# Kernel tuning notes

Measured on AMD Instinct MI355X. Metric: run time of the kernel, lower is better.

Reference implementation:

```python
import jax, jax.numpy as jnp
import numpy as np
import math

BATCH, SEQ, HIDDEN, HEADS = 2, 2048, 1024, 16
HEAD_SIZE = HIDDEN // HEADS
NEG_INF = -10000.0  # faithful to the torch module's masking constant


def setup_inputs() -> dict:
    key = jax.random.key(0)
    k1, k2, k3, k4 = jax.random.split(key, 4)
    x = jax.random.normal(k1, (BATCH, SEQ, HIDDEN), dtype=jnp.float32)
    pos_table = jax.random.normal(k2, (SEQ, HIDDEN), dtype=jnp.float32) * 0.02
    # torch nn.Linear weight layout: [out_features, in_features]
    Wqkv = jax.random.normal(k3, (3 * HIDDEN, HIDDEN), dtype=jnp.float32) * (1.0 / math.sqrt(HIDDEN))
    Wout = jax.random.normal(k4, (HIDDEN, HIDDEN), dtype=jnp.float32) * (1.0 / math.sqrt(HIDDEN))
    return {"x": x, "pos_table": pos_table, "Wqkv": Wqkv, "Wout": Wout}


def reference(x, pos_table, Wqkv, Wout):
    b, n, h = x.shape
    # positional embedding added for Q/K projection only (V uses raw x)
    xp = x + pos_table[None, :n, :]
    qk = jnp.einsum('bnd,ed->bne', xp, Wqkv[: 2 * HIDDEN])          # [b, n, 2h]
    q, k = jnp.split(qk, 2, axis=-1)
    v = jnp.einsum('bnd,ed->bne', x, Wqkv[2 * HIDDEN:])             # [b, n, h]

    def to_heads(t):  # b n (h l) -> b h n l
        return t.reshape(b, n, HEADS, HEAD_SIZE).transpose(0, 2, 1, 3)

    q, k, v = to_heads(q), to_heads(k), to_heads(v)

    scores = jnp.einsum('bhql,bhkl->bhqk', q, k) / math.sqrt(HEAD_SIZE)
    q_ind = jnp.arange(n)[:, None]
    k_ind = jnp.arange(n)[None, :]
    mask = q_ind < k_ind                                            # True where future
    scores = jnp.where(mask, NEG_INF, scores)
    probs = jax.nn.softmax(scores, axis=-1)
    combined_v = jnp.einsum('bhqk,bhkl->bhql', probs, v)            # [b, h, n, l]
    combined_v = combined_v.transpose(0, 2, 1, 3).reshape(b, n, h)  # b h q l -> b q (h l)
    out = jnp.einsum('bnd,ed->bne', combined_v, Wout)
    return out
```

## Files before the change

kernel.cpp:

```cpp
#include <hip/hip_runtime.h>
#include <hip/hip_bf16.h>
#include <stdint.h>

#define BATCH 2
#define SEQ   2048
#define HID   1024
#define NHEAD 16
#define HD    64
#define MROWS (BATCH*SEQ)

typedef __attribute__((ext_vector_type(8))) short bf16x8;
typedef __attribute__((ext_vector_type(4))) float f32x4;

__device__ inline unsigned pk2(float a, float b){
  __hip_bfloat162 h = __float22bfloat162_rn(make_float2(a, b));
  union { __hip_bfloat162 h; unsigned u; } v; v.h = h;
  return v.u;
}
__device__ inline float fexp2(float x){
#if __has_builtin(__builtin_amdgcn_exp2f)
  return __builtin_amdgcn_exp2f(x);
#else
  return exp2f(x);
#endif
}
__device__ inline void lds_load16(const short* g, short* l){
  __builtin_amdgcn_global_load_lds(
      (const __attribute__((address_space(1))) void*)g,
      (__attribute__((address_space(3))) void*)l, 16, 0, 0);
}

__global__ __launch_bounds__(256) void cast_xpos(
    const float* __restrict__ x, const float* __restrict__ pos,
    short* __restrict__ xb, short* __restrict__ xv){
  int i = blockIdx.x * 256 + threadIdx.x;
  float4 xa = ((const float4*)x)[i];
  float4 pa = ((const float4*)pos)[i & (SEQ*HID/4 - 1)];
  uint2 sb, sv;
  sb.x = pk2(xa.x + pa.x, xa.y + pa.y);
  sb.y = pk2(xa.z + pa.z, xa.w + pa.w);
  sv.x = pk2(xa.x, xa.y);
  sv.y = pk2(xa.z, xa.w);
  ((uint2*)xb)[i] = sb;
  ((uint2*)xv)[i] = sv;
}

__global__ __launch_bounds__(256) void cast_w2(
    const float* __restrict__ w1, const float* __restrict__ w2,
    short* __restrict__ o1, short* __restrict__ o2){
  int i = blockIdx.x * 256 + threadIdx.x;
  const int n1 = 3*HID*HID/4;
  const float4* src; uint2* dst; int j;
  if (i < n1){ src = (const float4*)w1; dst = (uint2*)o1; j = i; }
  else       { src = (const float4*)w2; dst = (uint2*)o2; j = i - n1; }
  float4 a = src[j];
  uint2 s;
  s.x = pk2(a.x, a.y);
  s.y = pk2(a.z, a.w);
  dst[j] = s;
}

template<bool F32OUT>
__global__ __launch_bounds__(256) void gemm_bt(
    const short* __restrict__ A0, const short* __restrict__ A1, int split_bx,
    const short* __restrict__ W, void* __restrict__ Cout, int K, int ldc,
    int qsb, float qscale){
  __shared__ alignas(16) short As[2][128*32];
  __shared__ alignas(16) short Bs[2][128*32];
  const int bx = blockIdx.x, by = blockIdx.y;
  const short* A = (bx < split_bx) ? A0 : A1;
  const int tid  = threadIdx.x;
  const int w    = tid >> 6, lane = tid & 63;
  const int g    = lane >> 4, c = lane & 15;
  const int wr   = w >> 1, wc = w & 1;

  f32x4 acc[4][4];
#pragma unroll
  for (int m = 0; m < 4; ++m)
#pragma unroll
    for (int n = 0; n < 4; ++n) acc[m][n] = (f32x4){0.f, 0.f, 0.f, 0.f};

  const short* Abase = A + (size_t)(by*128) * K;
  const short* Wbase = W + (size_t)(bx*128) * K;

  auto stage = [&](int buf, int kt){
#pragma unroll
    for (int j = 0; j < 2; ++j){
      int ci  = w*128 + j*64 + lane;
      int row = ci >> 2, sub = ci & 3;
      lds_load16(Abase + (size_t)row*K + kt + sub*8, &As[buf][(w*128 + j*64)*8]);
      lds_load16(Wbase + (size_t)row*K + kt + sub*8, &Bs[buf][(w*128 + j*64)*8]);
    }
  };

  const int nk = K >> 5;
  stage(0, 0);
  int buf = 0;
  for (int ki = 0; ki < nk; ++ki){
    __syncthreads();
    if (ki + 1 < nk) stage(buf ^ 1, (ki + 1) * 32);

    bf16x8 af[4], bfr[4];
#pragma unroll
    for (int m = 0; m < 4; ++m)
      af[m] = *(const bf16x8*)&As[buf][(wr*64 + m*16 + c)*32 + g*8];
#pragma unroll
    for (int n = 0; n < 4; ++n)
      bfr[n] = *(const bf16x8*)&Bs[buf][(wc*64 + n*16 + c)*32 + g*8];
    __builtin_amdgcn_s_setprio(1);
#pragma unroll
    for (int m = 0; m < 4; ++m)
#pragma unroll
      for (int n = 0; n < 4; ++n)
        acc[m][n] = __builtin_amdgcn_mfma_f32_16x16x32_bf16(af[m], bfr[n], acc[m][n], 0, 0, 0);
    __builtin_amdgcn_s_setprio(0);
    buf ^= 1;
  }

  const float sc = (bx < qsb) ? qscale : 1.0f;
  const int row0 = by*128 + wr*64;
  const int col0 = bx*128 + wc*64;
#pragma unroll
  for (int m = 0; m < 4; ++m)
#pragma unroll
    for (int n = 0; n < 4; ++n){
      size_t base = (size_t)(row0 + m*16 + g*4) * ldc + (col0 + n*16 + c);
      if constexpr (F32OUT){
#pragma unroll
        for (int r = 0; r < 4; ++r)
          ((float*)Cout)[base + (size_t)r*ldc] = acc[m][n][r] * sc;
      } else {
        short* p = (short*)Cout + base;
        unsigned u01 = pk2(acc[m][n][0]*sc, acc[m][n][1]*sc);
        unsigned u23 = pk2(acc[m][n][2]*sc, acc[m][n][3]*sc);
        p[0]             = (short)(u01 & 0xffff);
        p[(size_t)ldc]   = (short)(u01 >> 16);
        p[2*(size_t)ldc] = (short)(u23 & 0xffff);
        p[3*(size_t)ldc] = (short)(u23 >> 16);
      }
    }
}

__global__ __launch_bounds__(256) void attn_fwd(
    const short* __restrict__ qkv, short* __restrict__ out){
  const int bid = blockIdx.x;
  const int qt  = 15 - (bid >> 5);
  const int bh  = bid & 31;
  const int b   = bh >> 4, h = bh & 15;
  const int tid = threadIdx.x;
  const int w   = tid >> 6, lane = tid & 63;
  const int g   = lane >> 4, c = lane & 15;

  __shared__ alignas(16) short Ks[2][64*64];
  __shared__ alignas(16) short Vt[2][64*64];

  const int q0 = qt*128 + w*32;
  const size_t rowb = (size_t)b * SEQ;

  const short* qptrA = qkv + (rowb + q0 + c)*3072 + h*HD;
  const short* qptrB = qptrA + 16*3072;
  bf16x8 qfA0 = *(const bf16x8*)(qptrA + g*8);
  bf16x8 qfA1 = *(const bf16x8*)(qptrA + 32 + g*8);
  bf16x8 qfB0 = *(const bf16x8*)(qptrB + g*8);
  bf16x8 qfB1 = *(const bf16x8*)(qptrB + 32 + g*8);

  const short* kbase = qkv + rowb*3072 + HID   + h*HD;
  const short* vbase = qkv + rowb*3072 + 2*HID + h*HD;

  const int slot   = ((lane >> 5) << 5) | (((lane >> 2) & 3) << 3)
                   | (((lane >> 4) & 1) << 2) | (lane & 3);
  const int vchunk = slot >> 3, vcol = slot & 7;

  auto stageK = [&](int buf, int c0){
#pragma unroll
    for (int j = 0; j < 2; ++j){
      int pc  = w*128 + j*64 + lane;
      int row = pc >> 3;
      int lc  = (pc & 7) ^ (row & 7);
      lds_load16(kbase + (size_t)(c0 + row)*3072 + lc*8, &Ks[buf][(w*128 + j*64)*8]);
    }
  };
  auto loadV = [&](int c0, bf16x8& v0, bf16x8& v1){
    const short* vp = vbase + (size_t)(c0 + lane)*3072 + w*16;
    v0 = *(const bf16x8*)(vp);
    v1 = *(const bf16x8*)(vp + 8);
  };
  auto scatterV = [&](int buf, const bf16x8& v0, const bf16x8& v1){
#pragma unroll
    for (int j = 0; j < 8; ++j)
      Vt[buf][(w*16 + j)*64 + ((vchunk ^ (j & 7)) << 3) + vcol] = v0[j];
#pragma unroll
    for (int j = 0; j < 8; ++j)
      Vt[buf][(w*16 + 8 + j)*64 + ((vchunk ^ ((8 + j) & 7)) << 3) + vcol] = v1[j];
  };

  f32x4 otA[4], otB[4];
#pragma unroll
  for (int dt = 0; dt < 4; ++dt){
    otA[dt] = (f32x4){0.f, 0.f, 0.f, 0.f};
    otB[dt] = (f32x4){0.f, 0.f, 0.f, 0.f};
  }
  float mA = -1e30f, lA = 0.f, mB = -1e30f, lB = 0.f;
  const int qgA = q0 + c, qgB = q0 + 16 + c;

  {
    bf16x8 v0, v1;
    stageK(0, 0);
    loadV(0, v0, v1);
    scatterV(0, v0, v1);
  }
  int cur = 0;
  const int nch = 2*qt + 2;
  for (int ch = 0; ch < nch; ++ch){
    const int c0 = ch * 64;
    __syncthreads();

    bf16x8 nv0, nv1;
    if (ch + 1 < nch){
      stageK(cur ^ 1, c0 + 64);
      loadV(c0 + 64, nv0, nv1);
    }

    if (c0 <= q0 + 31){
      f32x4 sA[4], sB[4];
      __builtin_amdgcn_s_setprio(1);
#pragma unroll
      for (int kt = 0; kt < 4; ++kt){
        int row = kt*16 + c;
        bf16x8 k0 = *(const bf16x8*)&Ks[cur][row*64 + ((g       ^ (row&7))<<3)];
        bf16x8 k1 = *(const bf16x8*)&Ks[cur][row*64 + (((4 + g) ^ (row&7))<<3)];
        f32x4 z = (f32x4){0.f, 0.f, 0.f, 0.f};
        sA[kt] = __builtin_amdgcn_mfma_f32_16x16x32_bf16(k0, qfA0, z, 0, 0, 0);
        sA[kt] = __builtin_amdgcn_mfma_f32_16x16x32_bf16(k1, qfA1, sA[kt], 0, 0, 0);
        sB[kt] = __builtin_amdgcn_mfma_f32_16x16x32_bf16(k0, qfB0, z, 0, 0, 0);
        sB[kt] = __builtin_amdgcn_mfma_f32_16x16x32_bf16(k1, qfB1, sB[kt], 0, 0, 0);
      }
      __builtin_amdgcn_s_setprio(0);

      float pa[16], pb[16];
#pragma unroll
      for (int kt = 0; kt < 4; ++kt)
#pragma unroll
        for (int r = 0; r < 4; ++r){
          pa[kt*4 + r] = sA[kt][r];
          pb[kt*4 + r] = sB[kt][r];
        }

      if (ch >= nch - 2){
#pragma unroll
        for (int kt = 0; kt < 4; ++kt)
#pragma unroll
          for (int r = 0; r < 4; ++r){
            int ki = c0 + kt*16 + g*4 + r;
            if (ki > qgA) pa[kt*4 + r] = -1e30f;
            if (ki > qgB) pb[kt*4 + r] = -1e30f;
          }
      }

      float cmA = fmaxf(fmaxf(fmaxf(pa[0], pa[1]),  fmaxf(pa[2],  pa[3])),
                        fmaxf(fmaxf(pa[4], pa[5]),  fmaxf(pa[6],  pa[7])));
      cmA = fmaxf(cmA, fmaxf(fmaxf(fmaxf(pa[8],  pa[9]),  fmaxf(pa[10], pa[11])),
                             fmaxf(fmaxf(pa[12], pa[13]), fmaxf(pa[14], pa[15]))));
      float cmB = fmaxf(fmaxf(fmaxf(pb[0], pb[1]),  fmaxf(pb[2],  pb[3])),
                        fmaxf(fmaxf(pb[4], pb[5]),  fmaxf(pb[6],  pb[7])));
      cmB = fmaxf(cmB, fmaxf(fmaxf(fmaxf(pb[8],  pb[9]),  fmaxf(pb[10], pb[11])),
                             fmaxf(fmaxf(pb[12], pb[13]), fmaxf(pb[14], pb[15]))));
      cmA = fmaxf(cmA, __shfl_xor(cmA, 16));
      cmA = fmaxf(cmA, __shfl_xor(cmA, 32));
      cmB = fmaxf(cmB, __shfl_xor(cmB, 16));
      cmB = fmaxf(cmB, __shfl_xor(cmB, 32));
      if (__any(cmA > mA + 8.0f)){
        float mnew  = fmaxf(mA, cmA);
        float alpha = fexp2(mA - mnew);
        lA *= alpha;
#pragma unroll
        for (int dt = 0; dt < 4; ++dt)
#pragma unroll
          for (int r = 0; r < 4; ++r) otA[dt][r] *= alpha;
        mA = mnew;
      }
      if (__any(cmB > mB + 8.0f)){
        float mnew  = fmaxf(mB, cmB);
        float alpha = fexp2(mB - mnew);
        lB *= alpha;
#pragma unroll
        for (int dt = 0; dt < 4; ++dt)
#pragma unroll
          for (int r = 0; r < 4; ++r) otB[dt][r] *= alpha;
        mB = mnew;
      }
      float psA = 0.f, psB = 0.f;
#pragma unroll
      for (int i = 0; i < 16; ++i){
        pa[i] = fexp2(pa[i] - mA); psA += pa[i];
        pb[i] = fexp2(pb[i] - mB); psB += pb[i];
      }
      psA += __shfl_xor(psA, 16); psA += __shfl_xor(psA, 32);
      psB += __shfl_xor(psB, 16); psB += __shfl_xor(psB, 32);
      lA += psA; lB += psB;

      union { unsigned u[4]; bf16x8 v; } pA0, pA1, pB0, pB1;
      pA0.u[0] = pk2(pa[0],  pa[1]);  pA0.u[1] = pk2(pa[2],  pa[3]);
      pA0.u[2] = pk2(pa[4],  pa[5]);  pA0.u[3] = pk2(pa[6],  pa[7]);
      pA1.u[0] = pk2(pa[8],  pa[9]);  pA1.u[1] = pk2(pa[10], pa[11]);
      pA1.u[2] = pk2(pa[12], pa[13]); pA1.u[3] = pk2(pa[14], pa[15]);
      pB0.u[0] = pk2(pb[0],  pb[1]);  pB0.u[1] = pk2(pb[2],  pb[3]);
      pB0.u[2] = pk2(pb[4],  pb[5]);  pB0.u[3] = pk2(pb[6],  pb[7]);
      pB1.u[0] = pk2(pb[8],  pb[9]);  pB1.u[1] = pk2(pb[10], pb[11]);
      pB1.u[2] = pk2(pb[12], pb[13]); pB1.u[3] = pk2(pb[14], pb[15]);

      __builtin_amdgcn_s_setprio(1);
#pragma unroll
      for (int dt = 0; dt < 4; ++dt){
        int d = dt*16 + c;
        bf16x8 va0 = *(const bf16x8*)&Vt[cur][d*64 + ((g       ^ (d&7))<<3)];
        bf16x8 va1 = *(const bf16x8*)&Vt[cur][d*64 + (((4 + g) ^ (d&7))<<3)];
        otA[dt] = __builtin_amdgcn_mfma_f32_16x16x32_bf16(va0, pA0.v, otA[dt], 0, 0, 0);
        otA[dt] = __builtin_amdgcn_mfma_f32_16x16x32_bf16(va1, pA1.v, otA[dt], 0, 0, 0);
        otB[dt] = __builtin_amdgcn_mfma_f32_16x16x32_bf16(va0, pB0.v, otB[dt], 0, 0, 0);
        otB[dt] = __builtin_amdgcn_mfma_f32_16x16x32_bf16(va1, pB1.v, otB[dt], 0, 0, 0);
      }
      __builtin_amdgcn_s_setprio(0);
    }

    if (ch + 1 < nch) scatterV(cur ^ 1, nv0, nv1);
    cur ^= 1;
  }

  float invA = 1.f / lA, invB = 1.f / lB;
  short* obA = out + (rowb + q0 + c)*HID + h*HD + g*4;
  short* obB = obA + 16*HID;
#pragma unroll
  for (int dt = 0; dt < 4; ++dt){
    uint2 ua, ub;
    ua.x = pk2(otA[dt][0]*invA, otA[dt][1]*invA);
    ua.y = pk2(otA[dt][2]*invA, otA[dt][3]*invA);
    ub.x = pk2(otB[dt][0]*invB, otB[dt][1]*invB);
    ub.y = pk2(otB[dt][2]*invB, otB[dt][3]*invB);
    *(uint2*)(obA + dt*16) = ua;
    *(uint2*)(obB + dt*16) = ub;
  }
}

extern "C" void kernel_launch(void* const* d_in, const int* in_sizes, int n_in,
                              void* d_out, int out_size, void* d_ws, size_t ws_size,
                              hipStream_t stream){
  const float* x    = (const float*)d_in[0];
  const float* pos  = (const float*)d_in[1];
  const float* Wqkv = (const float*)d_in[2];
  const float* Wout = (const float*)d_in[3];

  short* xb     = (short*)d_ws;
  short* xv     = xb    + (size_t)MROWS*HID;
  short* wqkvb  = xv    + (size_t)MROWS*HID;
  short* woutb  = wqkvb + (size_t)3*HID*HID;
  short* qkv    = woutb + (size_t)HID*HID;
  short* attn_o = xb;

  cast_xpos<<<dim3(MROWS*HID/1024), 256, 0, stream>>>(x, pos, xb, xv);
  cast_w2<<<dim3(4*HID*HID/1024), 256, 0, stream>>>(Wqkv, Wout, wqkvb, woutb);

  gemm_bt<false><<<dim3(24, 32), 256, 0, stream>>>(xb, xv, 16, wqkvb, qkv, HID, 3*HID,
                                                   8, 0.18033688011112042f);

  attn_fwd<<<dim3(512), 256, 0, stream>>>(qkv, attn_o);

  gemm_bt<true><<<dim3(8, 32), 256, 0, stream>>>(attn_o, attn_o, 8, woutb, d_out, HID, HID,
                                                 0, 1.0f);
}
```

Before: 213.0 us.

## Split attention KV range across two wave halves, drop online max, remap GEMM grid

The two cast kernels are merged into one launch. Both GEMMs switch to a 1D grid with an XCD-aware block remap. Attention blocks now use 512 threads, with each half processing a balanced share of KV chunks and the halves combined through LDS at the end. The running-max rescaling is removed and replaced by a fixed -16 offset in the score accumulator, which removes max reductions and rescale work but relies on the scores staying bounded for numerical safety.

```diff
diff --git a/kernel.cpp b/kernel.cpp
--- a/kernel.cpp
+++ b/kernel.cpp
@@ -30,44 +30,49 @@
       (__attribute__((address_space(3))) void*)l, 16, 0, 0);
 }
 
-__global__ __launch_bounds__(256) void cast_xpos(
+__global__ __launch_bounds__(256) void cast_all(
     const float* __restrict__ x, const float* __restrict__ pos,
-    short* __restrict__ xb, short* __restrict__ xv){
-  int i = blockIdx.x * 256 + threadIdx.x;
-  float4 xa = ((const float4*)x)[i];
-  float4 pa = ((const float4*)pos)[i & (SEQ*HID/4 - 1)];
-  uint2 sb, sv;
-  sb.x = pk2(xa.x + pa.x, xa.y + pa.y);
-  sb.y = pk2(xa.z + pa.z, xa.w + pa.w);
-  sv.x = pk2(xa.x, xa.y);
-  sv.y = pk2(xa.z, xa.w);
-  ((uint2*)xb)[i] = sb;
-  ((uint2*)xv)[i] = sv;
-}
-
-__global__ __launch_bounds__(256) void cast_w2(
     const float* __restrict__ w1, const float* __restrict__ w2,
+    short* __restrict__ xb, short* __restrict__ xv,
     short* __restrict__ o1, short* __restrict__ o2){
   int i = blockIdx.x * 256 + threadIdx.x;
-  const int n1 = 3*HID*HID/4;
-  const float4* src; uint2* dst; int j;
-  if (i < n1){ src = (const float4*)w1; dst = (uint2*)o1; j = i; }
-  else       { src = (const float4*)w2; dst = (uint2*)o2; j = i - n1; }
-  float4 a = src[j];
-  uint2 s;
-  s.x = pk2(a.x, a.y);
-  s.y = pk2(a.z, a.w);
-  dst[j] = s;
+  const int n0 = MROWS*HID/4;
+  if (i < n0){
+    float4 xa = ((const float4*)x)[i];
+    float4 pa = ((const float4*)pos)[i & (SEQ*HID/4 - 1)];
+    uint2 sb, sv;
+    sb.x = pk2(xa.x + pa.x, xa.y + pa.y);
+    sb.y = pk2(xa.z + pa.z, xa.w + pa.w);
+    sv.x = pk2(xa.x, xa.y);
+    sv.y = pk2(xa.z, xa.w);
+    ((uint2*)xb)[i] = sb;
+    ((uint2*)xv)[i] = sv;
+  } else {
+    int j = i - n0;
+    const int n1 = 3*HID*HID/4;
+    const float4* src; uint2* dst; int k;
+    if (j < n1){ src = (const float4*)w1; dst = (uint2*)o1; k = j; }
+    else       { src = (const float4*)w2; dst = (uint2*)o2; k = j - n1; }
+    float4 a = src[k];
+    uint2 s;
+    s.x = pk2(a.x, a.y);
+    s.y = pk2(a.z, a.w);
+    dst[k] = s;
+  }
 }
 
 template<bool F32OUT>
 __global__ __launch_bounds__(256) void gemm_bt(
     const short* __restrict__ A0, const short* __restrict__ A1, int split_bx,
     const short* __restrict__ W, void* __restrict__ Cout, int K, int ldc,
-    int qsb, float qscale){
+    int gx, int qsb, float qscale){
+  const int nwg  = gridDim.x;
+  const int q    = nwg >> 3;
+  const int wgid = (blockIdx.x % 8) * q + (blockIdx.x / 8);
+  const int bx = wgid % gx, by = wgid / gx;
+
   __shared__ alignas(16) short As[2][128*32];
   __shared__ alignas(16) short Bs[2][128*32];
-  const int bx = blockIdx.x, by = blockIdx.y;
   const short* A = (bx < split_bx) ? A0 : A1;
   const int tid  = threadIdx.x;
   const int w    = tid >> 6, lane = tid & 63;
@@ -141,20 +146,20 @@
     }
 }
 
-__global__ __launch_bounds__(256) void attn_fwd(
+__global__ __launch_bounds__(512, 4) void attn_fwd(
     const short* __restrict__ qkv, short* __restrict__ out){
   const int bid = blockIdx.x;
-  const int qt  = 15 - (bid >> 5);
+  const int s   = 15 - (bid >> 5);
   const int bh  = bid & 31;
   const int b   = bh >> 4, h = bh & 15;
   const int tid = threadIdx.x;
-  const int w   = tid >> 6, lane = tid & 63;
-  const int g   = lane >> 4, c = lane & 15;
-
-  __shared__ alignas(16) short Ks[2][64*64];
-  __shared__ alignas(16) short Vt[2][64*64];
-
-  const int q0 = qt*128 + w*32;
+  const int wv  = tid >> 6, w4 = wv & 3, hf = wv >> 2;
+  const int lane = tid & 63, g = lane >> 4, c = lane & 15;
+
+  __shared__ alignas(16) short Ks[2][2][64*64];
+  __shared__ alignas(16) short Vt[2][2][64*64];
+
+  const int q0 = s*128 + w4*32;
   const size_t rowb = (size_t)b * SEQ;
 
   const short* qptrA = qkv + (rowb + q0 + c)*3072 + h*HD;
@@ -174,24 +179,25 @@
   auto stageK = [&](int buf, int c0){
 #pragma unroll
     for (int j = 0; j < 2; ++j){
-      int pc  = w*128 + j*64 + lane;
+      int pc  = w4*128 + j*64 + lane;
       int row = pc >> 3;
       int lc  = (pc & 7) ^ (row & 7);
-      lds_load16(kbase + (size_t)(c0 + row)*3072 + lc*8, &Ks[buf][(w*128 + j*64)*8]);
+      lds_load16(kbase + (size_t)(c0 + row)*3072 + lc*8,
+                 &Ks[hf][buf][(w4*128 + j*64)*8]);
     }
   };
   auto loadV = [&](int c0, bf16x8& v0, bf16x8& v1){
-    const short* vp = vbase + (size_t)(c0 + lane)*3072 + w*16;
+    const short* vp = vbase + (size_t)(c0 + lane)*3072 + w4*16;
     v0 = *(const bf16x8*)(vp);
     v1 = *(const bf16x8*)(vp + 8);
   };
   auto scatterV = [&](int buf, const bf16x8& v0, const bf16x8& v1){
 #pragma unroll
     for (int j = 0; j < 8; ++j)
-      Vt[buf][(w*16 + j)*64 + ((vchunk ^ (j & 7)) << 3) + vcol] = v0[j];
+      Vt[hf][buf][(w4*16 + j)*64 + ((vchunk ^ (j & 7)) << 3) + vcol] = v0[j];
 #pragma unroll
     for (int j = 0; j < 8; ++j)
-      Vt[buf][(w*16 + 8 + j)*64 + ((vchunk ^ ((8 + j) & 7)) << 3) + vcol] = v1[j];
+      Vt[hf][buf][(w4*16 + 8 + j)*64 + ((vchunk ^ ((8 + j) & 7)) << 3) + vcol] = v1[j];
   };
 
   f32x4 otA[4], otB[4];
@@ -200,39 +206,41 @@
     otA[dt] = (f32x4){0.f, 0.f, 0.f, 0.f};
     otB[dt] = (f32x4){0.f, 0.f, 0.f, 0.f};
   }
-  float mA = -1e30f, lA = 0.f, mB = -1e30f, lB = 0.f;
+  float lrA = 0.f, lrB = 0.f;
   const int qgA = q0 + c, qgB = q0 + 16 + c;
+  const int dch = q0 >> 6;
+  const int base_ch = hf ? (s + 1) : 0;
 
   {
     bf16x8 v0, v1;
-    stageK(0, 0);
-    loadV(0, v0, v1);
+    stageK(0, base_ch*64);
+    loadV(base_ch*64, v0, v1);
     scatterV(0, v0, v1);
   }
   int cur = 0;
-  const int nch = 2*qt + 2;
-  for (int ch = 0; ch < nch; ++ch){
+  for (int i = 0; i <= s; ++i){
+    const int ch = base_ch + i;
     const int c0 = ch * 64;
     __syncthreads();
 
     bf16x8 nv0, nv1;
-    if (ch + 1 < nch){
+    if (i < s){
       stageK(cur ^ 1, c0 + 64);
       loadV(c0 + 64, nv0, nv1);
     }
 
-    if (c0 <= q0 + 31){
+    if (ch <= dch){
       f32x4 sA[4], sB[4];
+      const f32x4 zsh = (f32x4){-16.f, -16.f, -16.f, -16.f};
       __builtin_amdgcn_s_setprio(1);
 #pragma unroll
       for (int kt = 0; kt < 4; ++kt){
         int row = kt*16 + c;
-        bf16x8 k0 = *(const bf16x8*)&Ks[cur][row*64 + ((g       ^ (row&7))<<3)];
-        bf16x8 k1 = *(const bf16x8*)&Ks[cur][row*64 + (((4 + g) ^ (row&7))<<3)];
-        f32x4 z = (f32x4){0.f, 0.f, 0.f, 0.f};
-        sA[kt] = __builtin_amdgcn_mfma_f32_16x16x32_bf16(k0, qfA0, z, 0, 0, 0);
+        bf16x8 k0 = *(const bf16x8*)&Ks[hf][cur][row*64 + ((g       ^ (row&7))<<3)];
+        bf16x8 k1 = *(const bf16x8*)&Ks[hf][cur][row*64 + (((4 + g) ^ (row&7))<<3)];
+        sA[kt] = __builtin_amdgcn_mfma_f32_16x16x32_bf16(k0, qfA0, zsh, 0, 0, 0);
         sA[kt] = __builtin_amdgcn_mfma_f32_16x16x32_bf16(k1, qfA1, sA[kt], 0, 0, 0);
-        sB[kt] = __builtin_amdgcn_mfma_f32_16x16x32_bf16(k0, qfB0, z, 0, 0, 0);
+        sB[kt] = __builtin_amdgcn_mfma_f32_16x16x32_bf16(k0, qfB0, zsh, 0, 0, 0);
         sB[kt] = __builtin_amdgcn_mfma_f32_16x16x32_bf16(k1, qfB1, sB[kt], 0, 0, 0);
       }
       __builtin_amdgcn_s_setprio(0);
@@ -246,7 +254,7 @@
           pb[kt*4 + r] = sB[kt][r];
         }
 
-      if (ch >= nch - 2){
+      if (ch == dch){
 #pragma unroll
         for (int kt = 0; kt < 4; ++kt)
 #pragma unroll
@@ -257,47 +265,13 @@
           }
       }
 
-      float cmA = fmaxf(fmaxf(fmaxf(pa[0], pa[1]),  fmaxf(pa[2],  pa[3])),
-                        fmaxf(fmaxf(pa[4], pa[5]),  fmaxf(pa[6],  pa[7])));
-      cmA = fmaxf(cmA, fmaxf(fmaxf(fmaxf(pa[8],  pa[9]),  fmaxf(pa[10], pa[11])),
-                             fmaxf(fmaxf(pa[12], pa[13]), fmaxf(pa[14], pa[15]))));
-      float cmB = fmaxf(fmaxf(fmaxf(pb[0], pb[1]),  fmaxf(pb[2],  pb[3])),
-                        fmaxf(fmaxf(pb[4], pb[5]),  fmaxf(pb[6],  pb[7])));
-      cmB = fmaxf(cmB, fmaxf(fmaxf(fmaxf(pb[8],  pb[9]),  fmaxf(pb[10], pb[11])),
-                             fmaxf(fmaxf(pb[12], pb[13]), fmaxf(pb[14], pb[15]))));
-      cmA = fmaxf(cmA, __shfl_xor(cmA, 16));
-      cmA = fmaxf(cmA, __shfl_xor(cmA, 32));
-      cmB = fmaxf(cmB, __shfl_xor(cmB, 16));
-      cmB = fmaxf(cmB, __shfl_xor(cmB, 32));
-      if (__any(cmA > mA + 8.0f)){
-        float mnew  = fmaxf(mA, cmA);
-        float alpha = fexp2(mA - mnew);
-        lA *= alpha;
-#pragma unroll
-        for (int dt = 0; dt < 4; ++dt)
-#pragma unroll
-          for (int r = 0; r < 4; ++r) otA[dt][r] *= alpha;
-        mA = mnew;
-      }
-      if (__any(cmB > mB + 8.0f)){
-        float mnew  = fmaxf(mB, cmB);
-        float alpha = fexp2(mB - mnew);
-        lB *= alpha;
-#pragma unroll
-        for (int dt = 0; dt < 4; ++dt)
-#pragma unroll
-          for (int r = 0; r < 4; ++r) otB[dt][r] *= alpha;
-        mB = mnew;
-      }
       float psA = 0.f, psB = 0.f;
 #pragma unroll
-      for (int i = 0; i < 16; ++i){
-        pa[i] = fexp2(pa[i] - mA); psA += pa[i];
-        pb[i] = fexp2(pb[i] - mB); psB += pb[i];
-      }
-      psA += __shfl_xor(psA, 16); psA += __shfl_xor(psA, 32);
-      psB += __shfl_xor(psB, 16); psB += __shfl_xor(psB, 32);
-      lA += psA; lB += psB;
+      for (int i2 = 0; i2 < 16; ++i2){
+        pa[i2] = fexp2(pa[i2]); psA += pa[i2];
+        pb[i2] = fexp2(pb[i2]); psB += pb[i2];
+      }
+      lrA += psA; lrB += psB;
 
       union { unsigned u[4]; bf16x8 v; } pA0, pA1, pB0, pB1;
       pA0.u[0] = pk2(pa[0],  pa[1]);  pA0.u[1] = pk2(pa[2],  pa[3]);
@@ -313,8 +287,8 @@
 #pragma unroll
       for (int dt = 0; dt < 4; ++dt){
         int d = dt*16 + c;
-        bf16x8 va0 = *(const bf16x8*)&Vt[cur][d*64 + ((g       ^ (d&7))<<3)];
-        bf16x8 va1 = *(const bf16x8*)&Vt[cur][d*64 + (((4 + g) ^ (d&7))<<3)];
+        bf16x8 va0 = *(const bf16x8*)&Vt[hf][cur][d*64 + ((g       ^ (d&7))<<3)];
+        bf16x8 va1 = *(const bf16x8*)&Vt[hf][cur][d*64 + (((4 + g) ^ (d&7))<<3)];
         otA[dt] = __builtin_amdgcn_mfma_f32_16x16x32_bf16(va0, pA0.v, otA[dt], 0, 0, 0);
         otA[dt] = __builtin_amdgcn_mfma_f32_16x16x32_bf16(va1, pA1.v, otA[dt], 0, 0, 0);
         otB[dt] = __builtin_amdgcn_mfma_f32_16x16x32_bf16(va0, pB0.v, otB[dt], 0, 0, 0);
@@ -323,22 +297,52 @@
       __builtin_amdgcn_s_setprio(0);
     }
 
-    if (ch + 1 < nch) scatterV(cur ^ 1, nv0, nv1);
+    if (i < s) scatterV(cur ^ 1, nv0, nv1);
     cur ^= 1;
   }
 
-  float invA = 1.f / lA, invB = 1.f / lB;
-  short* obA = out + (rowb + q0 + c)*HID + h*HD + g*4;
-  short* obB = obA + 16*HID;
-#pragma unroll
-  for (int dt = 0; dt < 4; ++dt){
-    uint2 ua, ub;
-    ua.x = pk2(otA[dt][0]*invA, otA[dt][1]*invA);
-    ua.y = pk2(otA[dt][2]*invA, otA[dt][3]*invA);
-    ub.x = pk2(otB[dt][0]*invB, otB[dt][1]*invB);
-    ub.y = pk2(otB[dt][2]*invB, otB[dt][3]*invB);
-    *(uint2*)(obA + dt*16) = ua;
-    *(uint2*)(obB + dt*16) = ub;
+  __syncthreads();
+  float* CmbA = (float*)&Ks[0][0][0];
+  float* CmbB = (float*)&Vt[0][0][0];
+  if (hf){
+    float* pA = CmbA + (w4*64 + lane)*18;
+    float* pB = CmbB + (w4*64 + lane)*16;
+#pragma unroll
+    for (int dt = 0; dt < 4; ++dt)
+#pragma unroll
+      for (int r = 0; r < 4; ++r){
+        pA[dt*4 + r] = otA[dt][r];
+        pB[dt*4 + r] = otB[dt][r];
+      }
+    pA[16] = lrA; pA[17] = lrB;
+  }
+  __syncthreads();
+  if (!hf){
+    const float* pA = CmbA + (w4*64 + lane)*18;
+    const float* pB = CmbB + (w4*64 + lane)*16;
+#pragma unroll
+    for (int dt = 0; dt < 4; ++dt)
+#pragma unroll
+      for (int r = 0; r < 4; ++r){
+        otA[dt][r] += pA[dt*4 + r];
+        otB[dt][r] += pB[dt*4 + r];
+      }
+    lrA += pA[16]; lrB += pA[17];
+    lrA += __shfl_xor(lrA, 16); lrA += __shfl_xor(lrA, 32);
+    lrB += __shfl_xor(lrB, 16); lrB += __shfl_xor(lrB, 32);
+    float invA = 1.f / lrA, invB = 1.f / lrB;
+    short* obA = out + (rowb + q0 + c)*HID + h*HD + g*4;
+    short* obB = obA + 16*HID;
+#pragma unroll
+    for (int dt = 0; dt < 4; ++dt){
+      uint2 ua, ub;
+      ua.x = pk2(otA[dt][0]*invA, otA[dt][1]*invA);
+      ua.y = pk2(otA[dt][2]*invA, otA[dt][3]*invA);
+      ub.x = pk2(otB[dt][0]*invB, otB[dt][1]*invB);
+      ub.y = pk2(otB[dt][2]*invB, otB[dt][3]*invB);
+      *(uint2*)(obA + dt*16) = ua;
+      *(uint2*)(obB + dt*16) = ub;
+    }
   }
 }
 
@@ -357,14 +361,14 @@
   short* qkv    = woutb + (size_t)HID*HID;
   short* attn_o = xb;
 
-  cast_xpos<<<dim3(MROWS*HID/1024), 256, 0, stream>>>(x, pos, xb, xv);
-  cast_w2<<<dim3(4*HID*HID/1024), 256, 0, stream>>>(Wqkv, Wout, wqkvb, woutb);
-
-  gemm_bt<false><<<dim3(24, 32), 256, 0, stream>>>(xb, xv, 16, wqkvb, qkv, HID, 3*HID,
-                                                   8, 0.18033688011112042f);
-
-  attn_fwd<<<dim3(512), 256, 0, stream>>>(qkv, attn_o);
-
-  gemm_bt<true><<<dim3(8, 32), 256, 0, stream>>>(attn_o, attn_o, 8, woutb, d_out, HID, HID,
-                                                 0, 1.0f);
-}
+  cast_all<<<dim3(8192), 256, 0, stream>>>(x, pos, Wqkv, Wout,
+                                           xb, xv, wqkvb, woutb);
+
+  gemm_bt<false><<<dim3(768), 256, 0, stream>>>(xb, xv, 16, wqkvb, qkv, HID, 3*HID,
+                                                24, 8, 0.18033688011112042f);
+
+  attn_fwd<<<dim3(512), 512, 0, stream>>>(qkv, attn_o);
+
+  gemm_bt<true><<<dim3(256), 256, 0, stream>>>(attn_o, attn_o, 8, woutb, d_out, HID, HID,
+                                               8, 0, 1.0f);
+}
```

Result: no change. 216.9 us (+1.8%).
